# Optimization experiments

Hardware: AMD Instinct MI355X
Metric: run time of the kernel (lower is better)

The kernel has to match this reference:

```python
import jax, jax.numpy as jnp
import numpy as np


def setup_inputs() -> dict:
    key = jax.random.key(0)
    ks = jax.random.split(key, 6)
    B, N_IN, N_OUT, C_IN, C_OUT, S, NNZ = 16, 6250, 25000, 64, 64, 9, 75000
    x = jax.random.normal(ks[0], (B, N_IN, C_IN), dtype=jnp.float32)
    trans_values = jax.random.uniform(ks[1], (NNZ,), dtype=jnp.float32)
    trans_row = jax.random.randint(ks[2], (NNZ,), 0, N_OUT, dtype=jnp.int32)
    trans_col = jax.random.randint(ks[3], (NNZ,), 0, N_IN, dtype=jnp.int32)
    spiral_indices = jax.random.randint(ks[4], (N_OUT, S), 0, N_OUT, dtype=jnp.int32)
    # Linear(S*C_IN -> C_OUT), kaiming-ish scale
    W = jax.random.normal(ks[5], (S * C_IN, C_OUT), dtype=jnp.float32) * (1.0 / np.sqrt(S * C_IN))
    b = jnp.zeros((C_OUT,), dtype=jnp.float32)
    return {"x": x, "trans_values": trans_values, "trans_row": trans_row,
            "trans_col": trans_col, "spiral_indices": spiral_indices,
            "W": W, "b": b, "n_out": N_OUT}


def reference(x, trans_values, trans_row, trans_col, spiral_indices, W, b, n_out):
    B, N_in, C = x.shape
    # Pool: gather cols, scale by sparse values, scatter-add to rows
    gathered = x[:, trans_col, :] * trans_values[None, :, None]        # [B, nnz, C]
    pooled = jnp.zeros((B, n_out, C), x.dtype).at[:, trans_row].add(gathered)  # [B, n_out, C]
    # SpiralConv: gather spiral neighborhoods, flatten, linear
    S = spiral_indices.shape[1]
    feat = pooled[:, spiral_indices, :].reshape(B, n_out, S * C)       # [B, n_out, S*C]
    out = feat @ W + b                                                 # [B, n_out, C_out]
    return jax.nn.elu(out)
```

## Files before the change

kernel.cpp:

```cpp
#include <hip/hip_runtime.h>

#define B_     16
#define N_IN_  6250
#define N_OUT_ 25000
#define C_     64
#define S_     9
#define NNZ_   75000
#define MT2_   98

typedef __bf16 bf16x8 __attribute__((ext_vector_type(8)));
typedef float floatx4 __attribute__((ext_vector_type(4)));

__device__ inline void async_copy16(const void* g, void* l) {
    __builtin_amdgcn_global_load_lds(
        (const __attribute__((address_space(1))) void*)g,
        (__attribute__((address_space(3))) void*)l, 16, 0, 0);
}


__global__ void hist_kernel(const int* __restrict__ rows, int* __restrict__ counts, int nnz) {
    int i = blockIdx.x * blockDim.x + threadIdx.x;
    if (i < nnz) atomicAdd(&counts[rows[i]], 1);
}

__global__ void scan1_kernel(const int* __restrict__ counts, int* __restrict__ offsets,
                             int* __restrict__ bsum, int n) {
    __shared__ int wsum[16];
    int t = threadIdx.x;
    int wid = t >> 6, lane = t & 63;
    int i = blockIdx.x * 1024 + t;
    int v = (i < n) ? counts[i] : 0;
    int s = v;
    #pragma unroll
    for (int d = 1; d < 64; d <<= 1) {
        int u = __shfl_up(s, d, 64);
        if (lane >= d) s += u;
    }
    if (lane == 63) wsum[wid] = s;
    __syncthreads();
    if (wid == 0 && lane < 16) {
        int ws = wsum[lane];
        #pragma unroll
        for (int d = 1; d < 16; d <<= 1) {
            int u = __shfl_up(ws, d, 64);
            if (lane >= d) ws += u;
        }
        wsum[lane] = ws;
    }
    __syncthreads();
    int wave_off = (wid == 0) ? 0 : wsum[wid - 1];
    int incl = s + wave_off;
    if (i < n) offsets[i] = incl - v;
    if (t == 1023) bsum[blockIdx.x] = incl;
}

__global__ void scan2_kernel(int* __restrict__ bsum, int* __restrict__ offsets, int nblk, int n) {
    if (threadIdx.x == 0) {
        int t = 0;
        for (int i = 0; i < nblk; ++i) { int v = bsum[i]; bsum[i] = t; t += v; }
        offsets[n] = t;
    }
}

__global__ void scan3_kernel(int* __restrict__ offsets, const int* __restrict__ bsum,
                             int* __restrict__ cursor, int n) {
    int i = blockIdx.x * 1024 + threadIdx.x;
    if (i < n) {
        int o = offsets[i] + bsum[blockIdx.x];
        offsets[i] = o;
        cursor[i] = o;
    }
}

__global__ void fill_kernel(const int* __restrict__ rows, const int* __restrict__ cols,
                            const float* __restrict__ vals, int* __restrict__ cursor,
                            int* __restrict__ ecol, float* __restrict__ eval, int nnz) {
    int i = blockIdx.x * blockDim.x + threadIdx.x;
    if (i < nnz) {
        int p = atomicAdd(&cursor[rows[i]], 1);
        ecol[p] = cols[i];
        eval[p] = vals[i];
    }
}

__global__ __launch_bounds__(256) void pool_kernel(
        const float* __restrict__ x, const int* __restrict__ offsets,
        const int* __restrict__ ecol, const float* __restrict__ eval,
        __bf16* __restrict__ pooled) {
    int t = threadIdx.x;
    int wid = t >> 6, lane = t & 63;
    int row = blockIdx.x * 4 + wid;
    int b = lane >> 2;
    int cq = (lane & 3) << 4;
    int beg = offsets[row], end = offsets[row + 1];

    const float* xb = x + (size_t)b * N_IN_ * C_ + cq;
    floatx4 acc[4] = {};

    int col = 0; float v = 0.f;
    if (beg < end) { col = ecol[beg]; v = eval[beg]; }
    for (int k = beg; k < end; ++k) {
        int col2 = 0; float v2 = 0.f;
        if (k + 1 < end) { col2 = ecol[k + 1]; v2 = eval[k + 1]; }
        const floatx4* xp = reinterpret_cast<const floatx4*>(xb + (size_t)col * C_);
        #pragma unroll
        for (int j = 0; j < 4; ++j) acc[j] += xp[j] * v;
        col = col2; v = v2;
    }

    __bf16* op = pooled + ((size_t)b * N_OUT_ + row) * C_ + cq;
    bf16x8 o0, o1;
    #pragma unroll
    for (int j = 0; j < 4; ++j) {
        o0[j]     = (__bf16)acc[0][j];
        o0[j + 4] = (__bf16)acc[1][j];
        o1[j]     = (__bf16)acc[2][j];
        o1[j + 4] = (__bf16)acc[3][j];
    }
    *reinterpret_cast<bf16x8*>(op)     = o0;
    *reinterpret_cast<bf16x8*>(op + 8) = o1;
}

__global__ void convw_kernel(const float* __restrict__ W, __bf16* __restrict__ WtF) {
    int i = blockIdx.x * blockDim.x + threadIdx.x;
    if (i < 72 * 64 * 8) {
        int kb = i >> 9;
        int n  = (i >> 3) & 63;
        int j  = i & 7;
        WtF[i] = (__bf16)W[(kb * 8 + j) * 64 + n];
    }
}

__global__ __launch_bounds__(256, 2) void gemm_kernel(
        const __bf16* __restrict__ pooled, const int* __restrict__ spiral,
        const __bf16* __restrict__ WtF, const float* __restrict__ bias,
        float* __restrict__ out) {
    __shared__ __bf16 Bs[72 * 64 * 8];

    int bx = blockIdx.x;
    int xcd = bx & 7;
    int rr = bx >> 3;
    int half = (rr >= MT2_) ? 1 : 0;
    int mt = rr - half * MT2_;
    int b = xcd + 8 * half;

    int t = threadIdx.x;
    int wave = t >> 6, lane = t & 63;
    int quad = lane >> 4, l16 = lane & 15;
    int mbase = mt * 256 + wave * 64;

    #pragma unroll
    for (int j = 0; j < 18; ++j) {
        int idx = t + j * 256;
        async_copy16((const char*)WtF + (size_t)idx * 16, (char*)Bs + idx * 16);
    }

    int src[4][S_];
    #pragma unroll
    for (int mi = 0; mi < 4; ++mi) {
        int m = mbase + mi * 16 + l16;
        int mc = (m < N_OUT_) ? m : 0;
        const int* sp = spiral + (size_t)mc * S_;
        int4 a0 = *reinterpret_cast<const int4*>(sp);
        int4 a1 = *reinterpret_cast<const int4*>(sp + 4);
        src[mi][0] = a0.x; src[mi][1] = a0.y; src[mi][2] = a0.z; src[mi][3] = a0.w;
        src[mi][4] = a1.x; src[mi][5] = a1.y; src[mi][6] = a1.z; src[mi][7] = a1.w;
        src[mi][8] = sp[8];
    }
    const __bf16* poolb = pooled + (size_t)b * N_OUT_ * C_;

    __syncthreads();

    floatx4 acc[4][4] = {};
    bf16x8 Acur[4][2], Anxt[4][2];

    auto loadA = [&](int s, bf16x8 (*A)[2]) {
        #pragma unroll
        for (int mi = 0; mi < 4; ++mi) {
            const __bf16* p = poolb + (size_t)src[mi][s] * C_ + quad * 8;
            A[mi][0] = *reinterpret_cast<const bf16x8*>(p);
            A[mi][1] = *reinterpret_cast<const bf16x8*>(p + 32);
        }
    };

    loadA(0, Acur);
    #pragma unroll
    for (int s = 0; s < S_; ++s) {
        if (s + 1 < S_) {
            loadA(s + 1, (s & 1) ? Acur : Anxt);
            __builtin_amdgcn_sched_barrier(0);
        }
        bf16x8 (*A)[2] = (s & 1) ? Anxt : Acur;
        #pragma unroll
        for (int kc = 0; kc < 2; ++kc) {
            #pragma unroll
            for (int nt = 0; nt < 4; ++nt) {
                int kb = s * 8 + kc * 4 + quad;
                bf16x8 bb = *reinterpret_cast<const bf16x8*>(
                    Bs + (((kb << 6) + (nt << 4) + l16) << 3));
                #pragma unroll
                for (int mi = 0; mi < 4; ++mi)
                    acc[mi][nt] = __builtin_amdgcn_mfma_f32_16x16x32_bf16(
                        A[mi][kc], bb, acc[mi][nt], 0, 0, 0);
            }
        }
    }

    float* outb = out + (size_t)b * N_OUT_ * C_;
    #pragma unroll
    for (int mi = 0; mi < 4; ++mi) {
        #pragma unroll
        for (int nt = 0; nt < 4; ++nt) {
            float bn = bias[nt * 16 + l16];
            #pragma unroll
            for (int i = 0; i < 4; ++i) {
                int mm = mbase + mi * 16 + quad * 4 + i;
                if (mm < N_OUT_) {
                    float v = acc[mi][nt][i] + bn;
                    v = (v > 0.0f) ? v : expm1f(v);
                    outb[(size_t)mm * C_ + nt * 16 + l16] = v;
                }
            }
        }
    }
}

extern "C" void kernel_launch(void* const* d_in, const int* in_sizes, int n_in,
                              void* d_out, int out_size, void* d_ws, size_t ws_size,
                              hipStream_t stream) {
    const float* x      = (const float*)d_in[0];
    const float* tvals  = (const float*)d_in[1];
    const int*   trow   = (const int*)d_in[2];
    const int*   tcol   = (const int*)d_in[3];
    const int*   spiral = (const int*)d_in[4];
    const float* W      = (const float*)d_in[5];
    const float* bias   = (const float*)d_in[6];
    float* out = (float*)d_out;

    char* ws = (char*)d_ws;
    size_t off = 0;
    auto alloc = [&](size_t bytes) -> void* {
        void* p = ws + off;
        off += (bytes + 255) & ~(size_t)255;
        return p;
    };
    __bf16* pooled  = (__bf16*)alloc((size_t)B_ * N_OUT_ * C_ * 2);
    __bf16* WtF     = (__bf16*)alloc(72 * 64 * 8 * 2);
    int*    cursor  = (int*)alloc(N_OUT_ * 4);
    int*    offsets = (int*)alloc((N_OUT_ + 1) * 4);
    int*    ecol    = (int*)alloc(NNZ_ * 4);
    float*  eval    = (float*)alloc(NNZ_ * 4);
    int*    counts  = (int*)alloc(N_OUT_ * 4);
    int*    bsum    = (int*)alloc(32 * 4);

    const int NBLK = (N_OUT_ + 1023) / 1024;
    hipMemsetAsync(counts, 0, N_OUT_ * 4, stream);
    hist_kernel<<<(NNZ_ + 255) / 256, 256, 0, stream>>>(trow, counts, NNZ_);
    scan1_kernel<<<NBLK, 1024, 0, stream>>>(counts, offsets, bsum, N_OUT_);
    scan2_kernel<<<1, 64, 0, stream>>>(bsum, offsets, NBLK, N_OUT_);
    scan3_kernel<<<NBLK, 1024, 0, stream>>>(offsets, bsum, cursor, N_OUT_);
    fill_kernel<<<(NNZ_ + 255) / 256, 256, 0, stream>>>(trow, tcol, tvals, cursor, ecol, eval, NNZ_);
    pool_kernel<<<N_OUT_ / 4, 256, 0, stream>>>(x, offsets, ecol, eval, pooled);
    convw_kernel<<<(72 * 64 * 8 + 255) / 256, 256, 0, stream>>>(W, WtF);
    gemm_kernel<<<8 * (2 * MT2_), 256, 0, stream>>>(pooled, spiral, WtF, bias, out);
}
```

Before: 288.3 us.

## Remap pool kernel blocks to XCD-local batches and deepen GEMM A prefetch

The pool kernel now assigns each block's low three bits (its XCD) to a pair of batches, so each XCD only touches x slices for two batches. Each lane handles two channels for two rows, which aims to improve L2 locality of the x gathers across MI355X's XCDs. The GEMM kernel moves from double-buffered to triple-buffered A register prefetch, loading two spiral steps ahead to hide gather latency. The cost is higher register pressure in the GEMM at 2 waves/SIMD, which may spill or limit occupancy. Each pool lane also does narrower float2 loads and serial work over two rows.

Result: slower. 311.4 us (+8.0%).

```diff
diff --git a/kernel.cpp b/kernel.cpp
--- a/kernel.cpp
+++ b/kernel.cpp
@@ -9,6 +9,7 @@
 #define MT2_   98
 
 typedef __bf16 bf16x8 __attribute__((ext_vector_type(8)));
+typedef __bf16 bf16x2 __attribute__((ext_vector_type(2)));
 typedef float floatx4 __attribute__((ext_vector_type(4)));
 
 __device__ inline void async_copy16(const void* g, void* l) {
@@ -87,38 +88,34 @@
         const float* __restrict__ x, const int* __restrict__ offsets,
         const int* __restrict__ ecol, const float* __restrict__ eval,
         __bf16* __restrict__ pooled) {
+    int bx = blockIdx.x;
+    int xcd = bx & 7;
+    int rg = bx >> 3;
     int t = threadIdx.x;
     int wid = t >> 6, lane = t & 63;
-    int row = blockIdx.x * 4 + wid;
-    int b = lane >> 2;
-    int cq = (lane & 3) << 4;
-    int beg = offsets[row], end = offsets[row + 1];
-
-    const float* xb = x + (size_t)b * N_IN_ * C_ + cq;
-    floatx4 acc[4] = {};
-
-    int col = 0; float v = 0.f;
-    if (beg < end) { col = ecol[beg]; v = eval[beg]; }
-    for (int k = beg; k < end; ++k) {
-        int col2 = 0; float v2 = 0.f;
-        if (k + 1 < end) { col2 = ecol[k + 1]; v2 = eval[k + 1]; }
-        const floatx4* xp = reinterpret_cast<const floatx4*>(xb + (size_t)col * C_);
-        #pragma unroll
-        for (int j = 0; j < 4; ++j) acc[j] += xp[j] * v;
-        col = col2; v = v2;
-    }
-
-    __bf16* op = pooled + ((size_t)b * N_OUT_ + row) * C_ + cq;
-    bf16x8 o0, o1;
-    #pragma unroll
-    for (int j = 0; j < 4; ++j) {
-        o0[j]     = (__bf16)acc[0][j];
-        o0[j + 4] = (__bf16)acc[1][j];
-        o1[j]     = (__bf16)acc[2][j];
-        o1[j + 4] = (__bf16)acc[3][j];
-    }
-    *reinterpret_cast<bf16x8*>(op)     = o0;
-    *reinterpret_cast<bf16x8*>(op + 8) = o1;
+    int b = xcd + 8 * (lane >> 5);
+    int c2 = (lane & 31) * 2;
+    const float* xb = x + (size_t)b * N_IN_ * C_ + c2;
+
+    #pragma unroll
+    for (int r = 0; r < 2; ++r) {
+        int row = rg * 8 + wid * 2 + r;
+        int beg = offsets[row], end = offsets[row + 1];
+        float ax = 0.f, ay = 0.f;
+        int col = 0; float v = 0.f;
+        if (beg < end) { col = ecol[beg]; v = eval[beg]; }
+        for (int k = beg; k < end; ++k) {
+            int col2 = 0; float v2 = 0.f;
+            if (k + 1 < end) { col2 = ecol[k + 1]; v2 = eval[k + 1]; }
+            const float2 xv = *reinterpret_cast<const float2*>(xb + (size_t)col * C_);
+            ax += xv.x * v;
+            ay += xv.y * v;
+            col = col2; v = v2;
+        }
+        bf16x2 o;
+        o[0] = (__bf16)ax; o[1] = (__bf16)ay;
+        *reinterpret_cast<bf16x2*>(pooled + ((size_t)b * N_OUT_ + row) * C_ + c2) = o;
+    }
 }
 
 __global__ void convw_kernel(const float* __restrict__ W, __bf16* __restrict__ WtF) {
@@ -172,7 +169,7 @@
     __syncthreads();
 
     floatx4 acc[4][4] = {};
-    bf16x8 Acur[4][2], Anxt[4][2];
+    bf16x8 A0[4][2], A1[4][2], A2[4][2];
 
     auto loadA = [&](int s, bf16x8 (*A)[2]) {
         #pragma unroll
@@ -183,14 +180,16 @@
         }
     };
 
-    loadA(0, Acur);
+    loadA(0, A0);
+    loadA(1, A1);
     #pragma unroll
     for (int s = 0; s < S_; ++s) {
-        if (s + 1 < S_) {
-            loadA(s + 1, (s & 1) ? Acur : Anxt);
+        if (s + 2 < S_) {
+            bf16x8 (*Apf)[2] = ((s + 2) % 3 == 0) ? A0 : (((s + 2) % 3 == 1) ? A1 : A2);
+            loadA(s + 2, Apf);
             __builtin_amdgcn_sched_barrier(0);
         }
-        bf16x8 (*A)[2] = (s & 1) ? Anxt : Acur;
+        bf16x8 (*A)[2] = (s % 3 == 0) ? A0 : ((s % 3 == 1) ? A1 : A2);
         #pragma unroll
         for (int kc = 0; kc < 2; ++kc) {
             #pragma unroll
@@ -260,7 +259,7 @@
     scan2_kernel<<<1, 64, 0, stream>>>(bsum, offsets, NBLK, N_OUT_);
     scan3_kernel<<<NBLK, 1024, 0, stream>>>(offsets, bsum, cursor, N_OUT_);
     fill_kernel<<<(NNZ_ + 255) / 256, 256, 0, stream>>>(trow, tcol, tvals, cursor, ecol, eval, NNZ_);
-    pool_kernel<<<N_OUT_ / 4, 256, 0, stream>>>(x, offsets, ecol, eval, pooled);
+    pool_kernel<<<8 * (N_OUT_ / 8), 256, 0, stream>>>(x, offsets, ecol, eval, pooled);
     convw_kernel<<<(72 * 64 * 8 + 255) / 256, 256, 0, stream>>>(W, WtF);
     gemm_kernel<<<8 * (2 * MT2_), 256, 0, stream>>>(pooled, spiral, WtF, bias, out);
 }
```

## Transpose to node-major batch-interleaved layout and stage spiral gathers through LDS

Applied to the files above, without the earlier changes.

A new transpose kernel rewrites x so that all 16 batches for one input node sit contiguously. The pool kernel then reads one contiguous 4 KB row per nonzero and writes pooled data node-major ([node][batch][channel]). The GEMM now processes 32 output nodes across all 16 batches per 512-thread block. It double-buffers each spiral neighbour's 2 KB row together with that step's W slice into LDS via async copies, using an XOR swizzle against bank conflicts. This is meant to replace scattered 16-byte global gathers with large contiguous ones and to share spiral indices across batches, at the cost of an extra transpose pass and heavier LDS use.

New measurement: 320.5 us. 11.2% more time.

```diff
diff --git a/kernel.cpp b/kernel.cpp
--- a/kernel.cpp
+++ b/kernel.cpp
@@ -6,9 +6,11 @@
 #define C_     64
 #define S_     9
 #define NNZ_   75000
-#define MT2_   98
+#define GM_    32
+#define NBLK_G 782
 
 typedef __bf16 bf16x8 __attribute__((ext_vector_type(8)));
+typedef __bf16 bf16x16 __attribute__((ext_vector_type(16)));
 typedef float floatx4 __attribute__((ext_vector_type(4)));
 
 __device__ inline void async_copy16(const void* g, void* l) {
@@ -83,42 +85,42 @@
     }
 }
 
+__global__ void transx_kernel(const float* __restrict__ x, float* __restrict__ xT) {
+    int n = blockIdx.x * 4 + (threadIdx.x >> 6);
+    int c = threadIdx.x & 63;
+    int b = blockIdx.y;
+    if (n < N_IN_)
+        xT[(size_t)n * 1024 + b * 64 + c] = x[(size_t)b * N_IN_ * C_ + (size_t)n * C_ + c];
+}
+
 __global__ __launch_bounds__(256) void pool_kernel(
-        const float* __restrict__ x, const int* __restrict__ offsets,
+        const float* __restrict__ xT, const int* __restrict__ offsets,
         const int* __restrict__ ecol, const float* __restrict__ eval,
-        __bf16* __restrict__ pooled) {
+        __bf16* __restrict__ pooledT) {
     int t = threadIdx.x;
     int wid = t >> 6, lane = t & 63;
     int row = blockIdx.x * 4 + wid;
-    int b = lane >> 2;
-    int cq = (lane & 3) << 4;
     int beg = offsets[row], end = offsets[row + 1];
 
-    const float* xb = x + (size_t)b * N_IN_ * C_ + cq;
     floatx4 acc[4] = {};
-
     int col = 0; float v = 0.f;
     if (beg < end) { col = ecol[beg]; v = eval[beg]; }
     for (int k = beg; k < end; ++k) {
         int col2 = 0; float v2 = 0.f;
         if (k + 1 < end) { col2 = ecol[k + 1]; v2 = eval[k + 1]; }
-        const floatx4* xp = reinterpret_cast<const floatx4*>(xb + (size_t)col * C_);
+        const floatx4* xp = reinterpret_cast<const floatx4*>(xT + (size_t)col * 1024 + lane * 16);
         #pragma unroll
         for (int j = 0; j < 4; ++j) acc[j] += xp[j] * v;
         col = col2; v = v2;
     }
 
-    __bf16* op = pooled + ((size_t)b * N_OUT_ + row) * C_ + cq;
-    bf16x8 o0, o1;
+    bf16x16 o;
     #pragma unroll
     for (int j = 0; j < 4; ++j) {
-        o0[j]     = (__bf16)acc[0][j];
-        o0[j + 4] = (__bf16)acc[1][j];
-        o1[j]     = (__bf16)acc[2][j];
-        o1[j + 4] = (__bf16)acc[3][j];
-    }
-    *reinterpret_cast<bf16x8*>(op)     = o0;
-    *reinterpret_cast<bf16x8*>(op + 8) = o1;
+        #pragma unroll
+        for (int jj = 0; jj < 4; ++jj) o[j * 4 + jj] = (__bf16)acc[j][jj];
+    }
+    *reinterpret_cast<bf16x16*>(pooledT + (size_t)row * 1024 + lane * 16) = o;
 }
 
 __global__ void convw_kernel(const float* __restrict__ W, __bf16* __restrict__ WtF) {
@@ -131,94 +133,108 @@
     }
 }
 
-__global__ __launch_bounds__(256, 2) void gemm_kernel(
-        const __bf16* __restrict__ pooled, const int* __restrict__ spiral,
+__global__ __launch_bounds__(512, 2) void gemm_kernel(
+        const __bf16* __restrict__ pooledT, const int* __restrict__ spiral,
         const __bf16* __restrict__ WtF, const float* __restrict__ bias,
         float* __restrict__ out) {
-    __shared__ __bf16 Bs[72 * 64 * 8];
+    __shared__ __bf16 As[2][GM_ * 1024];
+    __shared__ __bf16 Ws[2][4096];
+    __shared__ int spp[GM_][12];
 
     int bx = blockIdx.x;
-    int xcd = bx & 7;
-    int rr = bx >> 3;
-    int half = (rr >= MT2_) ? 1 : 0;
-    int mt = rr - half * MT2_;
-    int b = xcd + 8 * half;
-
+    int mbase = bx * GM_;
     int t = threadIdx.x;
     int wave = t >> 6, lane = t & 63;
-    int quad = lane >> 4, l16 = lane & 15;
-    int mbase = mt * 256 + wave * 64;
-
-    #pragma unroll
-    for (int j = 0; j < 18; ++j) {
-        int idx = t + j * 256;
-        async_copy16((const char*)WtF + (size_t)idx * 16, (char*)Bs + idx * 16);
-    }
-
-    int src[4][S_];
-    #pragma unroll
-    for (int mi = 0; mi < 4; ++mi) {
-        int m = mbase + mi * 16 + l16;
-        int mc = (m < N_OUT_) ? m : 0;
-        const int* sp = spiral + (size_t)mc * S_;
-        int4 a0 = *reinterpret_cast<const int4*>(sp);
-        int4 a1 = *reinterpret_cast<const int4*>(sp + 4);
-        src[mi][0] = a0.x; src[mi][1] = a0.y; src[mi][2] = a0.z; src[mi][3] = a0.w;
-        src[mi][4] = a1.x; src[mi][5] = a1.y; src[mi][6] = a1.z; src[mi][7] = a1.w;
-        src[mi][8] = sp[8];
-    }
-    const __bf16* poolb = pooled + (size_t)b * N_OUT_ * C_;
-
-    __syncthreads();
-
-    floatx4 acc[4][4] = {};
-    bf16x8 Acur[4][2], Anxt[4][2];
-
-    auto loadA = [&](int s, bf16x8 (*A)[2]) {
-        #pragma unroll
-        for (int mi = 0; mi < 4; ++mi) {
-            const __bf16* p = poolb + (size_t)src[mi][s] * C_ + quad * 8;
-            A[mi][0] = *reinterpret_cast<const bf16x8*>(p);
-            A[mi][1] = *reinterpret_cast<const bf16x8*>(p + 32);
-        }
+    int q = lane >> 4, l16 = lane & 15;
+
+    if (t < GM_ * S_) {
+        int r = t / S_, s = t - r * S_;
+        int m = mbase + r;
+        int mc = (m < N_OUT_) ? m : (N_OUT_ - 1);
+        spp[r][s] = spiral[mc * S_ + s];
+    }
+    __syncthreads();
+
+    auto stage = [&](int s, int d) {
+        #pragma unroll
+        for (int k = 0; k < 8; ++k) {
+            int c = t + k * 512;
+            int r = c >> 7;
+            int f = c & 127;
+            async_copy16((const char*)pooledT + (size_t)spp[r][s] * 2048
+                             + ((f ^ (r & 15)) << 4),
+                         (char*)&As[d][0] + ((size_t)c << 4));
+        }
+        async_copy16((const char*)WtF + (size_t)s * 8192 + ((size_t)t << 4),
+                     (char*)&Ws[d][0] + ((size_t)t << 4));
     };
 
-    loadA(0, Acur);
+    stage(0, 0);
+    __syncthreads();
+
+    floatx4 acc[2][2][4] = {};
+
     #pragma unroll
     for (int s = 0; s < S_; ++s) {
-        if (s + 1 < S_) {
-            loadA(s + 1, (s & 1) ? Acur : Anxt);
-            __builtin_amdgcn_sched_barrier(0);
-        }
-        bf16x8 (*A)[2] = (s & 1) ? Anxt : Acur;
-        #pragma unroll
-        for (int kc = 0; kc < 2; ++kc) {
+        int cur = s & 1;
+        if (s + 1 < S_) stage(s + 1, cur ^ 1);
+
+        bf16x8 wf[4][2];
+        #pragma unroll
+        for (int kc = 0; kc < 2; ++kc)
+            #pragma unroll
+            for (int nt = 0; nt < 4; ++nt)
+                wf[nt][kc] = *reinterpret_cast<const bf16x8*>(
+                    &Ws[cur][(((kc << 2) + q) << 6 | (nt << 4) | l16) << 3]);
+
+        bf16x8 af[2][2][2];
+        #pragma unroll
+        for (int bb = 0; bb < 2; ++bb) {
+            int bg = 2 * wave + bb;
+            #pragma unroll
+            for (int mi = 0; mi < 2; ++mi) {
+                int r = mi * 16 + l16;
+                #pragma unroll
+                for (int kc = 0; kc < 2; ++kc) {
+                    int F = (bg << 3) + (kc << 2) + q;
+                    af[bb][mi][kc] = *reinterpret_cast<const bf16x8*>(
+                        &As[cur][(size_t)r * 1024 + ((F ^ l16) << 3)]);
+                }
+            }
+        }
+
+        #pragma unroll
+        for (int kc = 0; kc < 2; ++kc)
+            #pragma unroll
+            for (int nt = 0; nt < 4; ++nt)
+                #pragma unroll
+                for (int bb = 0; bb < 2; ++bb)
+                    #pragma unroll
+                    for (int mi = 0; mi < 2; ++mi)
+                        acc[bb][mi][nt] = __builtin_amdgcn_mfma_f32_16x16x32_bf16(
+                            af[bb][mi][kc], wf[nt][kc], acc[bb][mi][nt], 0, 0, 0);
+
+        __syncthreads();
+    }
+
+    #pragma unroll
+    for (int bb = 0; bb < 2; ++bb) {
+        int bg = 2 * wave + bb;
+        float* outb = out + (size_t)bg * N_OUT_ * C_;
+        #pragma unroll
+        for (int mi = 0; mi < 2; ++mi) {
             #pragma unroll
             for (int nt = 0; nt < 4; ++nt) {
-                int kb = s * 8 + kc * 4 + quad;
-                bf16x8 bb = *reinterpret_cast<const bf16x8*>(
-                    Bs + (((kb << 6) + (nt << 4) + l16) << 3));
+                int col = (nt << 4) + l16;
+                float bn = bias[col];
                 #pragma unroll
-                for (int mi = 0; mi < 4; ++mi)
-                    acc[mi][nt] = __builtin_amdgcn_mfma_f32_16x16x32_bf16(
-                        A[mi][kc], bb, acc[mi][nt], 0, 0, 0);
-            }
-        }
-    }
-
-    float* outb = out + (size_t)b * N_OUT_ * C_;
-    #pragma unroll
-    for (int mi = 0; mi < 4; ++mi) {
-        #pragma unroll
-        for (int nt = 0; nt < 4; ++nt) {
-            float bn = bias[nt * 16 + l16];
-            #pragma unroll
-            for (int i = 0; i < 4; ++i) {
-                int mm = mbase + mi * 16 + quad * 4 + i;
-                if (mm < N_OUT_) {
-                    float v = acc[mi][nt][i] + bn;
-                    v = (v > 0.0f) ? v : expm1f(v);
-                    outb[(size_t)mm * C_ + nt * 16 + l16] = v;
+                for (int i = 0; i < 4; ++i) {
+                    int mm = mbase + mi * 16 + q * 4 + i;
+                    if (mm < N_OUT_) {
+                        float v = acc[bb][mi][nt][i] + bn;
+                        v = (v > 0.0f) ? v : expm1f(v);
+                        outb[(size_t)mm * C_ + col] = v;
+                    }
                 }
             }
         }
@@ -244,7 +260,8 @@
         off += (bytes + 255) & ~(size_t)255;
         return p;
     };
-    __bf16* pooled  = (__bf16*)alloc((size_t)B_ * N_OUT_ * C_ * 2);
+    __bf16* pooledT = (__bf16*)alloc((size_t)N_OUT_ * 16 * 64 * 2);
+    float*  xT      = (float*)alloc((size_t)N_IN_ * 16 * 64 * 4);
     __bf16* WtF     = (__bf16*)alloc(72 * 64 * 8 * 2);
     int*    cursor  = (int*)alloc(N_OUT_ * 4);
     int*    offsets = (int*)alloc((N_OUT_ + 1) * 4);
@@ -260,7 +277,8 @@
     scan2_kernel<<<1, 64, 0, stream>>>(bsum, offsets, NBLK, N_OUT_);
     scan3_kernel<<<NBLK, 1024, 0, stream>>>(offsets, bsum, cursor, N_OUT_);
     fill_kernel<<<(NNZ_ + 255) / 256, 256, 0, stream>>>(trow, tcol, tvals, cursor, ecol, eval, NNZ_);
-    pool_kernel<<<N_OUT_ / 4, 256, 0, stream>>>(x, offsets, ecol, eval, pooled);
+    transx_kernel<<<dim3((N_IN_ + 3) / 4, 16), 256, 0, stream>>>(x, xT);
     convw_kernel<<<(72 * 64 * 8 + 255) / 256, 256, 0, stream>>>(W, WtF);
-    gemm_kernel<<<8 * (2 * MT2_), 256, 0, stream>>>(pooled, spiral, WtF, bias, out);
-}
+    pool_kernel<<<N_OUT_ / 4, 256, 0, stream>>>(xT, offsets, ecol, eval, pooledT);
+    gemm_kernel<<<NBLK_G, 512, 0, stream>>>(pooledT, spiral, WtF, bias, out);
+}
```
